# Optimization experiments

Measured on AMD Instinct MI355X. Metric: run time of the kernel, lower is better.

The kernel has to match this reference:

```python
import jax, jax.numpy as jnp
from jax import lax
import numpy as np

T, B, I, H, E = 128, 64, 256, 512, 4
G = 4 * H  # gate width


def setup_inputs() -> dict:
    key = jax.random.key(0)
    ks = jax.random.split(key, 8)
    stdv = 1.0 / np.sqrt(H)
    x = jax.random.normal(ks[0], (T, B, I), dtype=jnp.float32)
    h0 = jax.random.normal(ks[1], (1, B, H), dtype=jnp.float32)
    c0 = jax.random.normal(ks[2], (1, B, H), dtype=jnp.float32)
    coef = jax.random.uniform(ks[3], (B, E), dtype=jnp.float32)
    Wi = jax.random.uniform(ks[4], (E, G, I), minval=-stdv, maxval=stdv, dtype=jnp.float32)
    bi = jax.random.uniform(ks[5], (E, G), minval=-stdv, maxval=stdv, dtype=jnp.float32)
    Wh = jax.random.uniform(ks[6], (E, G, H), minval=-stdv, maxval=stdv, dtype=jnp.float32)
    bh = jax.random.uniform(ks[7], (E, G), minval=-stdv, maxval=stdv, dtype=jnp.float32)
    return {"x": x, "h0": h0, "c0": c0, "coef": coef,
            "Wi": Wi, "bi": bi, "Wh": Wh, "bh": bh}


def reference(x, h0, c0, coef, Wi, bi, Wh, bh):
    # Expert input projections, combined with per-sample expert weights coef[B,E].
    # coef is time-invariant, so precompute the mixed input gates for all steps.
    xg = jnp.einsum('tbi,eoi->tbeo', x, Wi) + bi          # [T,B,E,4H]
    xg = jnp.einsum('be,tbeo->tbo', coef, xg)             # [T,B,4H]
    bhw = coef @ bh                                       # mixed hidden bias [B,4H]

    def step(carry, xg_t):
        h, c = carry                                      # [B,H]
        # mixture-of-experts hidden projection
        hg = jnp.einsum('bh,eoh->beo', h, Wh)             # [B,E,4H]
        hg = jnp.einsum('be,beo->bo', coef, hg)           # [B,4H]
        g = xg_t + hg + bhw
        i_g, f_g, c_g, o_g = jnp.split(g, 4, axis=-1)
        i_g = jax.nn.sigmoid(i_g)
        f_g = jax.nn.sigmoid(f_g)
        c_g = jnp.tanh(c_g)
        o_g = jax.nn.sigmoid(o_g)
        c = f_g * c + i_g * c_g
        h = o_g * jnp.tanh(c)
        return (h, c), h

    (h, c), out = lax.scan(step, (h0[0], c0[0]), xg)
    return out, h[None], c[None]
```

## Files before the change

### kernel.cpp

```cpp
#include <hip/hip_runtime.h>
#include <hip/hip_bf16.h>

typedef __hip_bfloat16 bf16;
typedef __attribute__((ext_vector_type(8))) short bf16x8;
typedef __attribute__((ext_vector_type(4))) short bf16x4;
typedef __attribute__((ext_vector_type(4))) float f32x4;
typedef __attribute__((ext_vector_type(2))) unsigned long long u64x2;

#define T_STEPS 128
#define NWG 256
#define NFLAGS 512
#define ZSLOTS 8

__device__ inline unsigned short f2bf(float f) {
    bf16 b = __float2bfloat16(f);
    return *reinterpret_cast<unsigned short*>(&b);
}


__global__ void prep_w2t(const float* __restrict__ Wh, bf16* __restrict__ W2T) {
    int idx = blockIdx.x * 256 + threadIdx.x;
    int o = idx >> 11, k = idx & 2047;
    int e = k >> 9, hh = k & 511;
    W2T[idx] = __float2bfloat16(Wh[((size_t)((e << 11) + o) << 9) + hh]);
}

__global__ void prep_w1t(const float* __restrict__ Wi, bf16* __restrict__ W1T) {
    int idx = blockIdx.x * 256 + threadIdx.x;
    int o = idx >> 10, k = idx & 1023;
    int e = k >> 8, i = k & 255;
    W1T[idx] = __float2bfloat16(Wi[((size_t)((e << 11) + o) << 8) + i]);
}

__global__ void prep_a1(const float* __restrict__ x, const float* __restrict__ coef,
                        bf16* __restrict__ A1) {
    int idx = blockIdx.x * 256 + threadIdx.x;
    int row = idx >> 10, k = idx & 1023;
    int b = row & 63;
    int e = k >> 8, i = k & 255;
    A1[idx] = __float2bfloat16(coef[(b << 2) + e] * x[((size_t)row << 8) + i]);
}

__global__ void prep_bias(const float* __restrict__ coef, const float* __restrict__ bi,
                          const float* __restrict__ bh, float* __restrict__ biasmix) {
    int idx = blockIdx.x * 256 + threadIdx.x;
    int b = idx >> 11, o = idx & 2047;
    float s = 0.f;
#pragma unroll
    for (int e = 0; e < 4; ++e)
        s += coef[(b << 2) + e] * (bi[(e << 11) + o] + bh[(e << 11) + o]);
    biasmix[idx] = s;
}

__global__ void prep_h0(const float* __restrict__ h0, bf16* __restrict__ hbuf,
                        unsigned* __restrict__ flags) {
    int idx = blockIdx.x * 256 + threadIdx.x;
    if (idx < NFLAGS) flags[idx] = 0u;
    int s = idx >> 9, u = idx & 511;
    int half = s >> 5, s32 = s & 31;
    int ug = u >> 2, uu = u & 3;
    hbuf[(size_t)half * (ZSLOTS * 16384) + ((ug << 5) + s32) * 4 + uu] =
        __float2bfloat16(h0[((size_t)s << 9) + u]);
}

__launch_bounds__(128, 1)
__global__ void lstm_rec(const bf16* __restrict__ W2T, const bf16* __restrict__ W1T,
                         const bf16* __restrict__ A1, const float* __restrict__ biasmix,
                         bf16* h_buf, const float* __restrict__ coef,
                         const float* __restrict__ c0, float* __restrict__ out,
                         unsigned* __restrict__ flags) {
    __shared__ bf16x8 W2L[4 * 16 * 64];
    __shared__ bf16x8 W1L[32 * 64];
    __shared__ unsigned hmail;

    const int wg   = blockIdx.x;
    const int half = wg >> 7;
    const int wgh  = wg & 127;
    const int j0   = wgh << 2;
    const int tid  = threadIdx.x;
    const int lane = tid & 63;
    const int wv   = tid >> 6;

    const int rlo  = lane & 15;
    const int kg   = lane >> 4;
    const int q    = rlo >> 2;
    const int jj   = rlo & 3;
    const int s32  = (wv << 4) + (kg << 2) + q;
    const int samp = (half << 5) + s32;
    const int arow = (half << 5) + (wv << 4) + rlo;
    const int a32  = (wv << 4) + rlo;
    const int o_ln = (q << 9) + j0 + jj;

    for (int g = tid; g < 4096; g += 128) {
        int e = g >> 10, kk = (g >> 6) & 15, l = g & 63;
        int rl = l & 15, kgg = l >> 4;
        int o = ((rl >> 2) << 9) + j0 + (rl & 3);
        W2L[g] = *(const bf16x8*)(W2T + ((size_t)o << 11) + (e << 9) + (kk << 5) + (kgg << 3));
    }
    for (int g = tid; g < 2048; g += 128) {
        int kk = g >> 6, l = g & 63;
        int rl = l & 15, kgg = l >> 4;
        int o = ((rl >> 2) << 9) + j0 + (rl & 3);
        W1L[g] = *(const bf16x8*)(W1T + ((size_t)o << 10) + (kk << 5) + (kgg << 3));
    }
    if (tid == 0) hmail = 0u;

    float bias_r[4];
    float4 cw[4];
#pragma unroll
    for (int r = 0; r < 4; ++r) {
        int row = (half << 5) + (wv << 4) + (kg << 2) + r;
        bias_r[r] = biasmix[((size_t)row << 11) + o_ln];
        cw[r] = *(const float4*)(coef + (row << 2));
    }
    float c_reg = c0[((size_t)samp << 9) + j0 + jj];

    bf16* hB = h_buf + (size_t)half * (ZSLOTS * 16384);
    unsigned* flagB = flags + (half << 8);

    __syncthreads();

    f32x4 acc0, acc1, acc2, acc3;
    {
        const bf16x8* xa = (const bf16x8*)A1 + ((size_t)arow << 7) + kg;
        acc0 = (f32x4){0.f, 0.f, 0.f, 0.f}; acc1 = acc0; acc2 = acc0; acc3 = acc0;
#pragma unroll
        for (int kk = 0; kk < 32; ++kk) {
            bf16x8 a = xa[kk << 2];
            bf16x8 b = W1L[(kk << 6) + lane];
            f32x4& ac = (kk & 3) == 0 ? acc0 : (kk & 3) == 1 ? acc1 : (kk & 3) == 2 ? acc2 : acc3;
            ac = __builtin_amdgcn_mfma_f32_16x16x32_bf16(a, b, ac, 0, 0, 0);
        }
    }

    float spin = 1.0f;

    for (int t = 0; t < T_STEPS; ++t) {
        if (t) {
            const unsigned tt = (unsigned)t;
            if (wv == 0) {
                const unsigned long long* f64 = (const unsigned long long*)flagB + (lane << 1);
                while (true) {
                    unsigned long long v0 = __hip_atomic_load(f64 + 0, __ATOMIC_RELAXED, __HIP_MEMORY_SCOPE_AGENT);
                    unsigned long long v1 = __hip_atomic_load(f64 + 1, __ATOMIC_RELAXED, __HIP_MEMORY_SCOPE_AGENT);
                    if ((unsigned)v0 >= tt && (unsigned)(v0 >> 32) >= tt &&
                        (unsigned)v1 >= tt && (unsigned)(v1 >> 32) >= tt) break;
#pragma unroll
                    for (int i = 0; i < 64; ++i)
                        spin = __builtin_fmaf(spin, 1.0000001f, 1e-30f);
                    asm volatile("" :: "v"(spin));
                }
                if (lane == 0)
                    __hip_atomic_store(&hmail, tt, __ATOMIC_RELEASE, __HIP_MEMORY_SCOPE_WORKGROUP);
            } else {
                while (__hip_atomic_load(&hmail, __ATOMIC_ACQUIRE, __HIP_MEMORY_SCOPE_WORKGROUP) < tt) {
#pragma unroll
                    for (int i = 0; i < 16; ++i)
                        spin = __builtin_fmaf(spin, 1.0000001f, 1e-30f);
                    asm volatile("" :: "v"(spin));
                }
            }
        }

        const bf16* hin  = hB + (((size_t)t & (ZSLOTS - 1)) << 14);
        bf16*       hout = hB + (((size_t)(t + 1) & (ZSLOTS - 1)) << 14);

        f32x4 e0 = {0.f, 0.f, 0.f, 0.f}, e1 = e0, e2 = e0, e3 = e0;
        {
            const unsigned long long* hq = (const unsigned long long*)hin;
            bf16x8 areg[16];
#pragma unroll
            for (int kk = 0; kk < 16; ++kk) {
                int ug = (kk << 3) + (kg << 1);
                unsigned long long lo = __hip_atomic_load(hq + (ug << 5) + a32,
                                                          __ATOMIC_RELAXED, __HIP_MEMORY_SCOPE_AGENT);
                unsigned long long hi = __hip_atomic_load(hq + ((ug + 1) << 5) + a32,
                                                          __ATOMIC_RELAXED, __HIP_MEMORY_SCOPE_AGENT);
                u64x2 t2; t2[0] = lo; t2[1] = hi;
                areg[kk] = __builtin_bit_cast(bf16x8, t2);
            }
#pragma unroll
            for (int kk = 0; kk < 16; ++kk) {
                e0 = __builtin_amdgcn_mfma_f32_16x16x32_bf16(areg[kk], W2L[(kk << 6) + lane       ], e0, 0, 0, 0);
                e1 = __builtin_amdgcn_mfma_f32_16x16x32_bf16(areg[kk], W2L[(kk << 6) + lane + 1024], e1, 0, 0, 0);
                e2 = __builtin_amdgcn_mfma_f32_16x16x32_bf16(areg[kk], W2L[(kk << 6) + lane + 2048], e2, 0, 0, 0);
                e3 = __builtin_amdgcn_mfma_f32_16x16x32_bf16(areg[kk], W2L[(kk << 6) + lane + 3072], e3, 0, 0, 0);
            }
        }

        f32x4 gv;
        {
            f32x4 xin = (acc0 + acc1) + (acc2 + acc3);
#pragma unroll
            for (int r = 0; r < 4; ++r)
                gv[r] = e0[r] * cw[r].x + e1[r] * cw[r].y + e2[r] * cw[r].z + e3[r] * cw[r].w
                      + xin[r] + bias_r[r];
        }

        const bool b0 = (q & 1), b1 = (q & 2);
        float own = b1 ? (b0 ? gv[3] : gv[2]) : (b0 ? gv[1] : gv[0]);
        float s1  = b1 ? (b0 ? gv[2] : gv[3]) : (b0 ? gv[0] : gv[1]);
        float s2  = b1 ? (b0 ? gv[1] : gv[0]) : (b0 ? gv[3] : gv[2]);
        float s3  = b1 ? (b0 ? gv[0] : gv[1]) : (b0 ? gv[2] : gv[3]);
        float r1 = __shfl_xor(s1, 4);
        float r2 = __shfl_xor(s2, 8);
        float r3 = __shfl_xor(s3, 12);
        float iG = (q == 0) ? own : (q == 1) ? r1 : (q == 2) ? r2 : r3;
        float fG = (q == 0) ? r1 : (q == 1) ? own : (q == 2) ? r3 : r2;
        float cG = (q == 0) ? r2 : (q == 1) ? r3 : (q == 2) ? own : r1;
        float oG = (q == 0) ? r3 : (q == 1) ? r2 : (q == 2) ? r1 : own;

        float ig = 1.f / (1.f + __expf(-iG));
        float fg = 1.f / (1.f + __expf(-fG));
        float cc = tanhf(cG);
        float og = 1.f / (1.f + __expf(-oG));
        float cn = fg * c_reg + ig * cc;
        float hv = og * tanhf(cn);
        c_reg = cn;

        unsigned u = (unsigned)f2bf(hv);
        unsigned w = (unsigned)__shfl_xor((int)u, 1);
        unsigned pair = (jj & 1) ? (w | (u << 16)) : (u | (w << 16));
        unsigned p2 = (unsigned)__shfl_xor((int)pair, 2);
        unsigned long long v64 = (jj & 2)
            ? ((unsigned long long)p2 | ((unsigned long long)pair << 32))
            : ((unsigned long long)pair | ((unsigned long long)p2 << 32));
        if (jj == 0)
            __hip_atomic_store((unsigned long long*)hout + (wgh << 5) + s32,
                               v64, __ATOMIC_RELAXED, __HIP_MEMORY_SCOPE_AGENT);

        asm volatile("s_waitcnt vmcnt(0)" ::: "memory");
        if (lane == 0)
            __hip_atomic_store(&flagB[(wgh << 1) + wv], (unsigned)(t + 1),
                               __ATOMIC_RELAXED, __HIP_MEMORY_SCOPE_AGENT);

        out[((size_t)t << 15) + ((size_t)samp << 9) + j0 + jj] = hv;
        if (t == T_STEPS - 1) {
            size_t base = (size_t)T_STEPS << 15;
            out[base + ((size_t)samp << 9) + j0 + jj] = hv;
            out[base + (1 << 15) + ((size_t)samp << 9) + j0 + jj] = cn;
        }
        if (t + 1 < T_STEPS) {
            const bf16x8* xa = (const bf16x8*)A1 + ((size_t)(((t + 1) << 6) + arow) << 7) + kg;
            acc0 = (f32x4){0.f, 0.f, 0.f, 0.f}; acc1 = acc0; acc2 = acc0; acc3 = acc0;
#pragma unroll
            for (int kk = 0; kk < 32; ++kk) {
                bf16x8 a = xa[kk << 2];
                bf16x8 b = W1L[(kk << 6) + lane];
                f32x4& ac = (kk & 3) == 0 ? acc0 : (kk & 3) == 1 ? acc1 : (kk & 3) == 2 ? acc2 : acc3;
                ac = __builtin_amdgcn_mfma_f32_16x16x32_bf16(a, b, ac, 0, 0, 0);
            }
        }
    }
}

extern "C" void kernel_launch(void* const* d_in, const int* in_sizes, int n_in,
                              void* d_out, int out_size, void* d_ws, size_t ws_size,
                              hipStream_t stream) {
    const float* x    = (const float*)d_in[0];
    const float* h0   = (const float*)d_in[1];
    const float* c0   = (const float*)d_in[2];
    const float* coef = (const float*)d_in[3];
    const float* Wi   = (const float*)d_in[4];
    const float* bi   = (const float*)d_in[5];
    const float* Wh   = (const float*)d_in[6];
    const float* bh   = (const float*)d_in[7];
    float* out = (float*)d_out;

    char* ws = (char*)d_ws;
    bf16*   W2T     = (bf16*)(ws);
    bf16*   W1T     = (bf16*)(ws + (8u  << 20));
    bf16*   A1      = (bf16*)(ws + (12u << 20));
    float*  biasmix = (float*)(ws + (28u << 20));
    bf16*   h_buf   = (bf16*)(ws + (28u << 20) + (512u << 10));
    unsigned* flags = (unsigned*)(ws + (29u << 20));

    prep_w2t <<<16384, 256, 0, stream>>>(Wh, W2T);
    prep_w1t <<< 8192, 256, 0, stream>>>(Wi, W1T);
    prep_a1  <<<32768, 256, 0, stream>>>(x, coef, A1);
    prep_bias<<<  512, 256, 0, stream>>>(coef, bi, bh, biasmix);
    prep_h0  <<<  128, 256, 0, stream>>>(h0, h_buf, flags);

    void* args[] = {(void*)&W2T, (void*)&W1T, (void*)&A1, (void*)&biasmix,
                    (void*)&h_buf, (void*)&coef, (void*)&c0, (void*)&out, (void*)&flags};
    hipLaunchCooperativeKernel((void*)lstm_rec, dim3(NWG), dim3(128), args, 0, stream);
}
```

Before: 754.2 us.

## Split batch into four independent wave groups to remove intra-workgroup mailbox sync

Each wave now owns its own 16-sample quarter of the batch, with separate h buffers and flag arrays per quarter. Each wave polls only the 128 flags of its own quarter directly, instead of wave 0 polling 256 flags and relaying through an LDS mailbox. This removes the two-level handoff and halves the number of flags each poller waits on. In exchange, every wave now polls global memory itself, which doubles the number of pollers.

Result: no change. 742.8 us (-1.5%).

```diff
diff --git a/kernel.cpp b/kernel.cpp
--- a/kernel.cpp
+++ b/kernel.cpp
@@ -3,7 +3,6 @@
 
 typedef __hip_bfloat16 bf16;
 typedef __attribute__((ext_vector_type(8))) short bf16x8;
-typedef __attribute__((ext_vector_type(4))) short bf16x4;
 typedef __attribute__((ext_vector_type(4))) float f32x4;
 typedef __attribute__((ext_vector_type(2))) unsigned long long u64x2;
 
@@ -57,9 +56,9 @@
     int idx = blockIdx.x * 256 + threadIdx.x;
     if (idx < NFLAGS) flags[idx] = 0u;
     int s = idx >> 9, u = idx & 511;
-    int half = s >> 5, s32 = s & 31;
+    int qt = s >> 4, s16 = s & 15;
     int ug = u >> 2, uu = u & 3;
-    hbuf[(size_t)half * (ZSLOTS * 16384) + ((ug << 5) + s32) * 4 + uu] =
+    hbuf[(size_t)qt * (ZSLOTS * 8192) + (((ug << 4) + s16) << 2) + uu] =
         __float2bfloat16(h0[((size_t)s << 9) + u]);
 }
 
@@ -71,24 +70,22 @@
                          unsigned* __restrict__ flags) {
     __shared__ bf16x8 W2L[4 * 16 * 64];
     __shared__ bf16x8 W1L[32 * 64];
-    __shared__ unsigned hmail;
 
     const int wg   = blockIdx.x;
-    const int half = wg >> 7;
     const int wgh  = wg & 127;
     const int j0   = wgh << 2;
     const int tid  = threadIdx.x;
     const int lane = tid & 63;
     const int wv   = tid >> 6;
+    const int qt   = ((wg >> 7) << 1) + wv;
 
     const int rlo  = lane & 15;
     const int kg   = lane >> 4;
     const int q    = rlo >> 2;
     const int jj   = rlo & 3;
-    const int s32  = (wv << 4) + (kg << 2) + q;
-    const int samp = (half << 5) + s32;
-    const int arow = (half << 5) + (wv << 4) + rlo;
-    const int a32  = (wv << 4) + rlo;
+    const int s16  = (kg << 2) + q;
+    const int samp = (qt << 4) + s16;
+    const int arow = (qt << 4) + rlo;
     const int o_ln = (q << 9) + j0 + jj;
 
     for (int g = tid; g < 4096; g += 128) {
@@ -103,20 +100,19 @@
         int o = ((rl >> 2) << 9) + j0 + (rl & 3);
         W1L[g] = *(const bf16x8*)(W1T + ((size_t)o << 10) + (kk << 5) + (kgg << 3));
     }
-    if (tid == 0) hmail = 0u;
 
     float bias_r[4];
     float4 cw[4];
 #pragma unroll
     for (int r = 0; r < 4; ++r) {
-        int row = (half << 5) + (wv << 4) + (kg << 2) + r;
+        int row = (qt << 4) + (kg << 2) + r;
         bias_r[r] = biasmix[((size_t)row << 11) + o_ln];
         cw[r] = *(const float4*)(coef + (row << 2));
     }
     float c_reg = c0[((size_t)samp << 9) + j0 + jj];
 
-    bf16* hB = h_buf + (size_t)half * (ZSLOTS * 16384);
-    unsigned* flagB = flags + (half << 8);
+    bf16* hB = h_buf + (size_t)qt * (ZSLOTS * 8192);
+    unsigned* flagB = flags + (qt << 7);
 
     __syncthreads();
 
@@ -137,33 +133,21 @@
 
     for (int t = 0; t < T_STEPS; ++t) {
         if (t) {
+            const unsigned long long* f64 = (const unsigned long long*)flagB + lane;
             const unsigned tt = (unsigned)t;
-            if (wv == 0) {
-                const unsigned long long* f64 = (const unsigned long long*)flagB + (lane << 1);
-                while (true) {
-                    unsigned long long v0 = __hip_atomic_load(f64 + 0, __ATOMIC_RELAXED, __HIP_MEMORY_SCOPE_AGENT);
-                    unsigned long long v1 = __hip_atomic_load(f64 + 1, __ATOMIC_RELAXED, __HIP_MEMORY_SCOPE_AGENT);
-                    if ((unsigned)v0 >= tt && (unsigned)(v0 >> 32) >= tt &&
-                        (unsigned)v1 >= tt && (unsigned)(v1 >> 32) >= tt) break;
-#pragma unroll
-                    for (int i = 0; i < 64; ++i)
-                        spin = __builtin_fmaf(spin, 1.0000001f, 1e-30f);
-                    asm volatile("" :: "v"(spin));
-                }
-                if (lane == 0)
-                    __hip_atomic_store(&hmail, tt, __ATOMIC_RELEASE, __HIP_MEMORY_SCOPE_WORKGROUP);
-            } else {
-                while (__hip_atomic_load(&hmail, __ATOMIC_ACQUIRE, __HIP_MEMORY_SCOPE_WORKGROUP) < tt) {
-#pragma unroll
-                    for (int i = 0; i < 16; ++i)
-                        spin = __builtin_fmaf(spin, 1.0000001f, 1e-30f);
-                    asm volatile("" :: "v"(spin));
-                }
-            }
-        }
-
-        const bf16* hin  = hB + (((size_t)t & (ZSLOTS - 1)) << 14);
-        bf16*       hout = hB + (((size_t)(t + 1) & (ZSLOTS - 1)) << 14);
+            while (true) {
+                unsigned long long v = __hip_atomic_load(f64, __ATOMIC_RELAXED,
+                                                         __HIP_MEMORY_SCOPE_AGENT);
+                if ((unsigned)v >= tt && (unsigned)(v >> 32) >= tt) break;
+#pragma unroll
+                for (int i = 0; i < 64; ++i)
+                    spin = __builtin_fmaf(spin, 1.0000001f, 1e-30f);
+                asm volatile("" :: "v"(spin));
+            }
+        }
+
+        const bf16* hin  = hB + (((size_t)t & (ZSLOTS - 1)) << 13);
+        bf16*       hout = hB + (((size_t)(t + 1) & (ZSLOTS - 1)) << 13);
 
         f32x4 e0 = {0.f, 0.f, 0.f, 0.f}, e1 = e0, e2 = e0, e3 = e0;
         {
@@ -172,9 +156,9 @@
 #pragma unroll
             for (int kk = 0; kk < 16; ++kk) {
                 int ug = (kk << 3) + (kg << 1);
-                unsigned long long lo = __hip_atomic_load(hq + (ug << 5) + a32,
+                unsigned long long lo = __hip_atomic_load(hq + (ug << 4) + rlo,
                                                           __ATOMIC_RELAXED, __HIP_MEMORY_SCOPE_AGENT);
-                unsigned long long hi = __hip_atomic_load(hq + ((ug + 1) << 5) + a32,
+                unsigned long long hi = __hip_atomic_load(hq + ((ug + 1) << 4) + rlo,
                                                           __ATOMIC_RELAXED, __HIP_MEMORY_SCOPE_AGENT);
                 u64x2 t2; t2[0] = lo; t2[1] = hi;
                 areg[kk] = __builtin_bit_cast(bf16x8, t2);
@@ -226,12 +210,12 @@
             ? ((unsigned long long)p2 | ((unsigned long long)pair << 32))
             : ((unsigned long long)pair | ((unsigned long long)p2 << 32));
         if (jj == 0)
-            __hip_atomic_store((unsigned long long*)hout + (wgh << 5) + s32,
+            __hip_atomic_store((unsigned long long*)hout + (wgh << 4) + s16,
                                v64, __ATOMIC_RELAXED, __HIP_MEMORY_SCOPE_AGENT);
 
         asm volatile("s_waitcnt vmcnt(0)" ::: "memory");
         if (lane == 0)
-            __hip_atomic_store(&flagB[(wgh << 1) + wv], (unsigned)(t + 1),
+            __hip_atomic_store(&flagB[wgh], (unsigned)(t + 1),
                                __ATOMIC_RELAXED, __HIP_MEMORY_SCOPE_AGENT);
 
         out[((size_t)t << 15) + ((size_t)samp << 9) + j0 + jj] = hv;
```
